# Kernel optimization log

Hardware: AMD Instinct MI355X
Metric: run time of the kernel (lower is better)

The kernel has to match this reference:

```python
import jax, jax.numpy as jnp
import numpy as np

N, K, D = 65536, 16, 64  # points, neighbors, d_out
EPS = 1e-5


def setup_inputs() -> dict:
    key = jax.random.key(0)
    ks = jax.random.split(key, 10)
    s = lambda fan: 1.0 / np.sqrt(fan)
    return {
        "p": jax.random.normal(ks[0], (N, K, 3), jnp.float32),
        "x": jax.random.normal(ks[1], (N, K, D), jnp.float32),
        # BiMLP: Conv1d(10, 2D, 1) -> BN -> ReLU -> Conv1d(2D, D, 1)
        "w1": jax.random.normal(ks[2], (10, 2 * D), jnp.float32) * s(10),
        "b1": jnp.zeros((2 * D,), jnp.float32),
        "g1": jnp.ones((2 * D,), jnp.float32),
        "be1": jnp.zeros((2 * D,), jnp.float32),
        "w2": jax.random.normal(ks[3], (2 * D, D), jnp.float32) * s(2 * D),
        "b2": jnp.zeros((D,), jnp.float32),
        # score_fn: Linear(2D, 2D, bias=False)
        "ws": jax.random.normal(ks[4], (2 * D, 2 * D), jnp.float32) * s(2 * D),
        # mlp_out: Linear(2D, D) -> BN -> ReLU
        "wo": jax.random.normal(ks[5], (2 * D, D), jnp.float32) * s(2 * D),
        "bo": jnp.zeros((D,), jnp.float32),
        "g2": jnp.ones((D,), jnp.float32),
        "be2": jnp.zeros((D,), jnp.float32),
    }


def reference(p, x, w1, b1, g1, be1, w2, b2, ws, wo, bo, g2, be2):
    # p: [N,K,3] neighbor coords (index 0 is the center), x: [N,K,D]
    center = p[:, :1, :]                                   # [N,1,3]
    diff = center - p                                      # [N,K,3]
    dist = jnp.sqrt(jnp.sum(diff * diff, axis=2, keepdims=True))  # [N,K,1]
    concat = jnp.concatenate(
        [jnp.broadcast_to(center, p.shape), p, diff, dist], axis=-1)  # [N,K,10]

    # 1x1 conv == per-point linear over channel dim
    h = jnp.einsum('nkc,cd->nkd', concat, w1) + b1          # [N,K,2D]
    # BatchNorm1d over (N,K) per channel (training-mode batch stats)
    mu = jnp.mean(h, axis=(0, 1))
    var = jnp.var(h, axis=(0, 1))
    h = (h - mu) * jax.lax.rsqrt(var + EPS) * g1 + be1
    h = jax.nn.relu(h)
    p_c = jnp.einsum('nkd,de->nke', h, w2) + b2             # [N,K,D]

    p_x = jnp.concatenate([p_c, x], axis=-1)                # [N,K,2D]
    # attention scores: linear (no bias) then softmax over neighbor dim (-2)
    scores = jax.nn.softmax(jnp.einsum('nkd,de->nke', p_x, ws), axis=-2)
    feat = jnp.sum(scores * p_x, axis=1)                    # [N,2D]

    out = feat @ wo + bo                                    # [N,D]
    mu2 = jnp.mean(out, axis=0)
    var2 = jnp.var(out, axis=0)
    out = (out - mu2) * jax.lax.rsqrt(var2 + EPS) * g2 + be2
    return jax.nn.relu(out)
```

## Files before the change

kernel.cpp:

```cpp
#include <hip/hip_runtime.h>
#include <math.h>

#define NPTS 65536
#define EPSV 1e-5f
#define B1G  256
#define B3G  512

#define OFF_P1  0
#define OFF_S1  (B1G*65)
#define OFF_P2  (OFF_S1+256)
#define OFF_S2  (OFF_P2+B3G*128)
#define OFF_PRE (OFF_S2+128)

typedef unsigned int u32;
typedef short v8s __attribute__((ext_vector_type(8)));
typedef float v4f __attribute__((ext_vector_type(4)));

union F8 { v8s v; u32 u[4]; unsigned short s[8]; };

__device__ __forceinline__ u32 f2bf(float f){
  u32 u = __float_as_uint(f);
  return (u + 0x7fffu + ((u>>16)&1u)) >> 16;
}
__device__ __forceinline__ float bf2f(unsigned short s){ return __uint_as_float(((u32)s)<<16); }
__device__ __forceinline__ u32 packbf(float a, float b){ return f2bf(a) | (f2bf(b)<<16); }

__global__ __launch_bounds__(256) void k1_stats(const float* __restrict__ p, float* __restrict__ part1){
  int tid = blockIdx.x*256 + threadIdx.x;
  float M[55]; float s[10];
  #pragma unroll
  for(int i=0;i<55;i++) M[i]=0.f;
  #pragma unroll
  for(int i=0;i<10;i++) s[i]=0.f;
  for(int it=0; it<16; ++it){
    int r = it*65536 + tid;
    int n = r >> 4;
    int kk = r & 15;
    const float* pn = p + (size_t)n*48;
    float cx=pn[0], cy=pn[1], cz=pn[2];
    float ax=pn[kk*3+0], ay=pn[kk*3+1], az=pn[kk*3+2];
    float dx=cx-ax, dy=cy-ay, dz=cz-az;
    float dd = sqrtf(dx*dx+dy*dy+dz*dz);
    float c[10]={cx,cy,cz,ax,ay,az,dx,dy,dz,dd};
    #pragma unroll
    for(int i=0;i<10;i++) s[i]+=c[i];
    int idx=0;
    #pragma unroll
    for(int i=0;i<10;i++){
      #pragma unroll
      for(int j=i;j<10;j++){
        M[idx] = fmaf(c[i],c[j],M[idx]);
        idx++;
      }
    }
  }
  #pragma unroll
  for(int i=0;i<10;i++){
    for(int off=32; off>0; off>>=1) s[i] += __shfl_down(s[i], off, 64);
  }
  #pragma unroll
  for(int i=0;i<55;i++){
    for(int off=32; off>0; off>>=1) M[i] += __shfl_down(M[i], off, 64);
  }
  __shared__ float sm[4][65];
  int lane = threadIdx.x & 63, w = threadIdx.x >> 6;
  if(lane==0){
    #pragma unroll
    for(int i=0;i<10;i++) sm[w][i]=s[i];
    #pragma unroll
    for(int i=0;i<55;i++) sm[w][10+i]=M[i];
  }
  __syncthreads();
  if(threadIdx.x<65){
    float v = sm[0][threadIdx.x]+sm[1][threadIdx.x]+sm[2][threadIdx.x]+sm[3][threadIdx.x];
    part1[blockIdx.x*65 + threadIdx.x] = v;
  }
}

__device__ __forceinline__ int tri_idx(int i,int j){
  int a = i<j? i : j;
  int b = i<j? j : i;
  return 10*a - (a*(a-1))/2 + (b-a);
}
__global__ void k2_fin(const float* __restrict__ part1, const float* __restrict__ w1,
                       const float* __restrict__ g1, const float* __restrict__ be1,
                       float* __restrict__ stats1){
  __shared__ float S[65];
  int t = threadIdx.x;
  if(t<65){
    float a=0.f;
    for(int b=0;b<B1G;b++) a += part1[b*65+t];
    S[t]=a;
  }
  __syncthreads();
  float wc[10];
  #pragma unroll
  for(int c=0;c<10;c++) wc[c]=w1[c*128+t];
  float md=0.f;
  #pragma unroll
  for(int c=0;c<10;c++) md += S[c]*wc[c];
  const float invR = 1.0f/(float)(NPTS*16);
  md *= invR;
  float q=0.f;
  #pragma unroll
  for(int i=0;i<10;i++){
    float ti=0.f;
    #pragma unroll
    for(int j=0;j<10;j++) ti += S[10+tri_idx(i,j)]*wc[j];
    q = fmaf(ti, wc[i], q);
  }
  q *= invR;
  float var = q - md*md;
  float sc = g1[t]*rsqrtf(var+EPSV);
  float sh = be1[t] - md*sc;
  stats1[t]=sc;
  stats1[128+t]=sh;
}

__global__ __launch_bounds__(256,2) void k3_main(
    const float* __restrict__ p, const float* __restrict__ x,
    const float* __restrict__ w2, const float* __restrict__ b2,
    const float* __restrict__ wsm, const float* __restrict__ wo,
    const float* __restrict__ w1, const float* __restrict__ stats1,
    float* __restrict__ pre, float* __restrict__ part2)
{
  __shared__ unsigned short s_h [4][16][136];
  __shared__ unsigned short s_px[4][16][136];
  __shared__ float          s_lg[4][16][132];
  __shared__ unsigned short s_ft[16][136];

  const int tid  = threadIdx.x;
  const int w    = tid>>6;
  const int lane = tid&63;
  const int q    = lane>>4;
  const int c    = lane&15;

  v8s Bw1[2], Bw2[4], Bws[2][4], Bwo[4];
  #pragma unroll
  for(int t=0;t<2;t++){
    F8 f;
    #pragma unroll
    for(int j=0;j<8;j++){
      int k = q*8+j;
      f.s[j] = (unsigned short)(k<10 ? f2bf(w1[k*128 + 32*w + 16*t + c]) : 0);
    }
    Bw1[t]=f.v;
  }
  #pragma unroll
  for(int kk=0;kk<4;kk++){
    F8 f;
    #pragma unroll
    for(int j=0;j<8;j++) f.s[j]=(unsigned short)f2bf(w2[(kk*32+q*8+j)*64 + 16*w + c]);
    Bw2[kk]=f.v;
  }
  #pragma unroll
  for(int t=0;t<2;t++){
    #pragma unroll
    for(int kk=0;kk<4;kk++){
      F8 f;
      #pragma unroll
      for(int j=0;j<8;j++) f.s[j]=(unsigned short)f2bf(wsm[(kk*32+q*8+j)*128 + 32*w + 16*t + c]);
      Bws[t][kk]=f.v;
    }
  }
  #pragma unroll
  for(int kk=0;kk<4;kk++){
    F8 f;
    #pragma unroll
    for(int j=0;j<8;j++) f.s[j]=(unsigned short)f2bf(wo[(kk*32+q*8+j)*64 + 16*w + c]);
    Bwo[kk]=f.v;
  }
  const float sc1a = stats1[32*w+c],    sh1a = stats1[128+32*w+c];
  const float sc1b = stats1[32*w+16+c], sh1b = stats1[128+32*w+16+c];
  const float b2v  = b2[16*w+c];

  float a_s=0.f, a_q=0.f;
  const int base0 = blockIdx.x*128;

  for(int r=0;r<32;++r){
    const int base = base0 + 4*r;

    const float4* xg = (const float4*)(x + (size_t)base*1024);
    #pragma unroll
    for(int rr=0;rr<4;rr++){
      int f = tid + 256*rr;
      float4 v = xg[f];
      int nl = f>>8, rem = f&255, pt = rem>>4, d4 = rem&15;
      *(uint2*)&s_px[nl][pt][64+4*d4] = make_uint2(packbf(v.x,v.y), packbf(v.z,v.w));
    }

    #pragma unroll
    for(int n0=0;n0<4;n0++){
      const float* pn = p + (size_t)(base+n0)*48;
      float cx=pn[0], cy=pn[1], cz=pn[2];
      float ax=pn[3*c], ay=pn[3*c+1], az=pn[3*c+2];
      float dx=cx-ax, dy=cy-ay, dz=cz-az;
      float dd=sqrtf(dx*dx+dy*dy+dz*dz);
      float cr[10]={cx,cy,cz,ax,ay,az,dx,dy,dz,dd};
      F8 fa;
      #pragma unroll
      for(int j=0;j<8;j++){ int k=q*8+j; fa.s[j]=(unsigned short)(k<10 ? f2bf(cr[k]) : 0); }
      v4f z={0.f,0.f,0.f,0.f};
      v4f d0 = __builtin_amdgcn_mfma_f32_16x16x32_bf16(fa.v, Bw1[0], z, 0,0,0);
      v4f d1 = __builtin_amdgcn_mfma_f32_16x16x32_bf16(fa.v, Bw1[1], z, 0,0,0);
      #pragma unroll
      for(int i=0;i<4;i++){
        float v0 = fmaxf(0.f, fmaf(d0[i], sc1a, sh1a));
        float v1 = fmaxf(0.f, fmaf(d1[i], sc1b, sh1b));
        s_h[n0][4*q+i][32*w+c]    = (unsigned short)f2bf(v0);
        s_h[n0][4*q+i][32*w+16+c] = (unsigned short)f2bf(v1);
      }
    }
    __syncthreads();

    #pragma unroll
    for(int n0=0;n0<4;n0++){
      const v8s* Ar = (const v8s*)&s_h[n0][c][0];
      v4f acc={0.f,0.f,0.f,0.f};
      #pragma unroll
      for(int kk=0;kk<4;kk++)
        acc = __builtin_amdgcn_mfma_f32_16x16x32_bf16(Ar[kk*4+q], Bw2[kk], acc, 0,0,0);
      #pragma unroll
      for(int i=0;i<4;i++) s_px[n0][4*q+i][16*w+c] = (unsigned short)f2bf(acc[i] + b2v);
    }
    __syncthreads();

    #pragma unroll
    for(int n0=0;n0<4;n0++){
      const v8s* Ar = (const v8s*)&s_px[n0][c][0];
      v4f l0={0.f,0.f,0.f,0.f}, l1={0.f,0.f,0.f,0.f};
      #pragma unroll
      for(int kk=0;kk<4;kk++){
        v8s a = Ar[kk*4+q];
        l0 = __builtin_amdgcn_mfma_f32_16x16x32_bf16(a, Bws[0][kk], l0, 0,0,0);
        l1 = __builtin_amdgcn_mfma_f32_16x16x32_bf16(a, Bws[1][kk], l1, 0,0,0);
      }
      #pragma unroll
      for(int i=0;i<4;i++){
        s_lg[n0][4*q+i][32*w+c]    = l0[i];
        s_lg[n0][4*q+i][32*w+16+c] = l1[i];
      }
    }
    __syncthreads();

    {
      const int slot = (r&3)*4 + w;
      #pragma unroll
      for(int hh=0;hh<2;hh++){
        const int ch = lane + 64*hh;
        float lv[16];
        #pragma unroll
        for(int pt=0;pt<16;pt++) lv[pt] = s_lg[w][pt][ch];
        float m = lv[0];
        #pragma unroll
        for(int pt=1;pt<16;pt++) m = fmaxf(m, lv[pt]);
        float se=0.f, fe=0.f;
        #pragma unroll
        for(int pt=0;pt<16;pt++){
          float e = __expf(lv[pt]-m);
          se += e;
          fe = fmaf(e, bf2f(s_px[w][pt][ch]), fe);
        }
        s_ft[slot][ch] = (unsigned short)f2bf(fe/se);
      }
    }
    __syncthreads();

    if((r&3)==3){
      const v8s* Ar = (const v8s*)&s_ft[c][0];
      v4f o={0.f,0.f,0.f,0.f};
      #pragma unroll
      for(int kk=0;kk<4;kk++)
        o = __builtin_amdgcn_mfma_f32_16x16x32_bf16(Ar[kk*4+q], Bwo[kk], o, 0,0,0);
      const int nb16 = base0 + (r>>2)*16;
      #pragma unroll
      for(int i=0;i<4;i++){
        float val = o[i];
        pre[(size_t)(nb16 + 4*q + i)*64 + 16*w + c] = val;
        a_s += val;
        a_q = fmaf(val,val,a_q);
      }
    }
  }

  a_s += __shfl_xor(a_s, 16, 64); a_s += __shfl_xor(a_s, 32, 64);
  a_q += __shfl_xor(a_q, 16, 64); a_q += __shfl_xor(a_q, 32, 64);
  if(q==0){
    part2[blockIdx.x*128 + 16*w + c]      = a_s;
    part2[blockIdx.x*128 + 64 + 16*w + c] = a_q;
  }
}

__global__ void k4_fin(const float* __restrict__ part2, const float* __restrict__ g2,
                       const float* __restrict__ be2, float* __restrict__ stats2){
  int t = threadIdx.x;
  float s=0.f, qq=0.f;
  for(int b=0;b<B3G;b++){ s += part2[b*128+t]; qq += part2[b*128+64+t]; }
  float mu  = s/(float)NPTS;
  float var = qq/(float)NPTS - mu*mu;
  float sc = g2[t]*rsqrtf(var+EPSV);
  float sh = be2[t] - mu*sc;
  stats2[t]=sc;
  stats2[64+t]=sh;
}

__global__ __launch_bounds__(256) void k5_apply(const float* __restrict__ pre,
                                                const float* __restrict__ stats2,
                                                float* __restrict__ out){
  int i = blockIdx.x*256 + threadIdx.x;
  float4 v = ((const float4*)pre)[i];
  int d4 = i & 15;
  float4 sc = ((const float4*)stats2)[d4];
  float4 sh = ((const float4*)(stats2+64))[d4];
  float4 o;
  o.x = fmaxf(0.f, fmaf(v.x,sc.x,sh.x));
  o.y = fmaxf(0.f, fmaf(v.y,sc.y,sh.y));
  o.z = fmaxf(0.f, fmaf(v.z,sc.z,sh.z));
  o.w = fmaxf(0.f, fmaf(v.w,sc.w,sh.w));
  ((float4*)out)[i] = o;
}

extern "C" void kernel_launch(void* const* d_in, const int* in_sizes, int n_in,
                              void* d_out, int out_size, void* d_ws, size_t ws_size,
                              hipStream_t stream){
  (void)in_sizes; (void)n_in; (void)out_size; (void)ws_size;
  const float* p   = (const float*)d_in[0];
  const float* x   = (const float*)d_in[1];
  const float* w1  = (const float*)d_in[2];
  const float* g1  = (const float*)d_in[4];
  const float* be1 = (const float*)d_in[5];
  const float* w2  = (const float*)d_in[6];
  const float* b2  = (const float*)d_in[7];
  const float* wsm = (const float*)d_in[8];
  const float* wo  = (const float*)d_in[9];
  const float* g2  = (const float*)d_in[11];
  const float* be2 = (const float*)d_in[12];

  float* wsf    = (float*)d_ws;
  float* part1  = wsf + OFF_P1;
  float* stats1 = wsf + OFF_S1;
  float* part2  = wsf + OFF_P2;
  float* stats2 = wsf + OFF_S2;
  float* pre    = wsf + OFF_PRE;
  float* out    = (float*)d_out;

  k1_stats<<<B1G,256,0,stream>>>(p, part1);
  k2_fin  <<<1,128,0,stream>>>(part1, w1, g1, be1, stats1);
  k3_main <<<B3G,256,0,stream>>>(p,x,w2,b2,wsm,wo,w1,stats1,pre,part2);
  k4_fin  <<<1,64,0,stream>>>(part2,g2,be2,stats2);
  k5_apply<<<4096,256,0,stream>>>(pre,stats2,out);
}
```

Measured before the change: 593.1 us.

## Fuse softmax into score MFMA epilogue, double k3 grid, parallelize finalize kernels

Softmax over neighbors is now computed directly from the MFMA score accumulators using cross-lane shuffles. This removes the float logit shared-memory buffer and one block barrier per iteration. The main kernel's grid doubles with half the points per block and a higher occupancy hint. Float-to-bf16 packing now uses the hardware v_cvt_pk_bf16_f32 instruction and division uses v_rcp_f32. Both reduction finalize kernels split their serial sums across more threads. Occupancy gains depend on register pressure fitting 4 blocks, and the fast reciprocal slightly changes rounding.

New measurement: 503.2 us. -15.1%, faster.

```diff
diff --git a/kernel.cpp b/kernel.cpp
--- a/kernel.cpp
+++ b/kernel.cpp
@@ -4,7 +4,7 @@
 #define NPTS 65536
 #define EPSV 1e-5f
 #define B1G  256
-#define B3G  512
+#define B3G  1024
 
 #define OFF_P1  0
 #define OFF_S1  (B1G*65)
@@ -23,7 +23,12 @@
   return (u + 0x7fffu + ((u>>16)&1u)) >> 16;
 }
 __device__ __forceinline__ float bf2f(unsigned short s){ return __uint_as_float(((u32)s)<<16); }
-__device__ __forceinline__ u32 packbf(float a, float b){ return f2bf(a) | (f2bf(b)<<16); }
+__device__ __forceinline__ u32 packbf(float a, float b){
+  u32 r; asm("v_cvt_pk_bf16_f32 %0, %1, %2" : "=v"(r) : "v"(a), "v"(b)); return r;
+}
+__device__ __forceinline__ float rcpf(float x){
+  float r; asm("v_rcp_f32 %0, %1" : "=v"(r) : "v"(x)); return r;
+}
 
 __global__ __launch_bounds__(256) void k1_stats(const float* __restrict__ p, float* __restrict__ part1){
   int tid = blockIdx.x*256 + threadIdx.x;
@@ -82,42 +87,48 @@
   int b = i<j? j : i;
   return 10*a - (a*(a-1))/2 + (b-a);
 }
-__global__ void k2_fin(const float* __restrict__ part1, const float* __restrict__ w1,
+__global__ __launch_bounds__(256) void k2_fin(const float* __restrict__ part1, const float* __restrict__ w1,
                        const float* __restrict__ g1, const float* __restrict__ be1,
                        float* __restrict__ stats1){
+  __shared__ float P[4][65];
   __shared__ float S[65];
   int t = threadIdx.x;
-  if(t<65){
+  for(int idx=t; idx<260; idx+=256){
+    int seg = idx/65, v = idx - seg*65;
     float a=0.f;
-    for(int b=0;b<B1G;b++) a += part1[b*65+t];
-    S[t]=a;
+    for(int b=seg; b<B1G; b+=4) a += part1[b*65+v];
+    P[seg][v]=a;
   }
   __syncthreads();
-  float wc[10];
-  #pragma unroll
-  for(int c=0;c<10;c++) wc[c]=w1[c*128+t];
-  float md=0.f;
-  #pragma unroll
-  for(int c=0;c<10;c++) md += S[c]*wc[c];
-  const float invR = 1.0f/(float)(NPTS*16);
-  md *= invR;
-  float q=0.f;
-  #pragma unroll
-  for(int i=0;i<10;i++){
-    float ti=0.f;
-    #pragma unroll
-    for(int j=0;j<10;j++) ti += S[10+tri_idx(i,j)]*wc[j];
-    q = fmaf(ti, wc[i], q);
-  }
-  q *= invR;
-  float var = q - md*md;
-  float sc = g1[t]*rsqrtf(var+EPSV);
-  float sh = be1[t] - md*sc;
-  stats1[t]=sc;
-  stats1[128+t]=sh;
-}
-
-__global__ __launch_bounds__(256,2) void k3_main(
+  if(t<65) S[t] = P[0][t]+P[1][t]+P[2][t]+P[3][t];
+  __syncthreads();
+  if(t<128){
+    float wc[10];
+    #pragma unroll
+    for(int c=0;c<10;c++) wc[c]=w1[c*128+t];
+    float md=0.f;
+    #pragma unroll
+    for(int c=0;c<10;c++) md += S[c]*wc[c];
+    const float invR = 1.0f/(float)(NPTS*16);
+    md *= invR;
+    float q=0.f;
+    #pragma unroll
+    for(int i=0;i<10;i++){
+      float ti=0.f;
+      #pragma unroll
+      for(int j=0;j<10;j++) ti += S[10+tri_idx(i,j)]*wc[j];
+      q = fmaf(ti, wc[i], q);
+    }
+    q *= invR;
+    float var = q - md*md;
+    float sc = g1[t]*rsqrtf(var+EPSV);
+    float sh = be1[t] - md*sc;
+    stats1[t]=sc;
+    stats1[128+t]=sh;
+  }
+}
+
+__global__ __launch_bounds__(256,4) void k3_main(
     const float* __restrict__ p, const float* __restrict__ x,
     const float* __restrict__ w2, const float* __restrict__ b2,
     const float* __restrict__ wsm, const float* __restrict__ wo,
@@ -126,7 +137,6 @@
 {
   __shared__ unsigned short s_h [4][16][136];
   __shared__ unsigned short s_px[4][16][136];
-  __shared__ float          s_lg[4][16][132];
   __shared__ unsigned short s_ft[16][136];
 
   const int tid  = threadIdx.x;
@@ -175,9 +185,9 @@
   const float b2v  = b2[16*w+c];
 
   float a_s=0.f, a_q=0.f;
-  const int base0 = blockIdx.x*128;
-
-  for(int r=0;r<32;++r){
+  const int base0 = blockIdx.x*64;
+
+  for(int r=0;r<16;++r){
     const int base = base0 + 4*r;
 
     const float4* xg = (const float4*)(x + (size_t)base*1024);
@@ -196,10 +206,13 @@
       float ax=pn[3*c], ay=pn[3*c+1], az=pn[3*c+2];
       float dx=cx-ax, dy=cy-ay, dz=cz-az;
       float dd=sqrtf(dx*dx+dy*dy+dz*dz);
-      float cr[10]={cx,cy,cz,ax,ay,az,dx,dy,dz,dd};
+      u32 pk01=packbf(cx,cy), pk23=packbf(cz,ax), pk45=packbf(ay,az),
+          pk67=packbf(dx,dy), pk89=packbf(dz,dd);
       F8 fa;
-      #pragma unroll
-      for(int j=0;j<8;j++){ int k=q*8+j; fa.s[j]=(unsigned short)(k<10 ? f2bf(cr[k]) : 0); }
+      fa.u[0] = q==0 ? pk01 : (q==1 ? pk89 : 0u);
+      fa.u[1] = q==0 ? pk23 : 0u;
+      fa.u[2] = q==0 ? pk45 : 0u;
+      fa.u[3] = q==0 ? pk67 : 0u;
       v4f z={0.f,0.f,0.f,0.f};
       v4f d0 = __builtin_amdgcn_mfma_f32_16x16x32_bf16(fa.v, Bw1[0], z, 0,0,0);
       v4f d1 = __builtin_amdgcn_mfma_f32_16x16x32_bf16(fa.v, Bw1[1], z, 0,0,0);
@@ -207,8 +220,9 @@
       for(int i=0;i<4;i++){
         float v0 = fmaxf(0.f, fmaf(d0[i], sc1a, sh1a));
         float v1 = fmaxf(0.f, fmaf(d1[i], sc1b, sh1b));
-        s_h[n0][4*q+i][32*w+c]    = (unsigned short)f2bf(v0);
-        s_h[n0][4*q+i][32*w+16+c] = (unsigned short)f2bf(v1);
+        u32 pk = packbf(v0, v1);
+        s_h[n0][4*q+i][32*w+c]    = (unsigned short)pk;
+        s_h[n0][4*q+i][32*w+16+c] = (unsigned short)(pk>>16);
       }
     }
     __syncthreads();
@@ -221,7 +235,11 @@
       for(int kk=0;kk<4;kk++)
         acc = __builtin_amdgcn_mfma_f32_16x16x32_bf16(Ar[kk*4+q], Bw2[kk], acc, 0,0,0);
       #pragma unroll
-      for(int i=0;i<4;i++) s_px[n0][4*q+i][16*w+c] = (unsigned short)f2bf(acc[i] + b2v);
+      for(int i=0;i<4;i+=2){
+        u32 pk = packbf(acc[i]+b2v, acc[i+1]+b2v);
+        s_px[n0][4*q+i][16*w+c]   = (unsigned short)pk;
+        s_px[n0][4*q+i+1][16*w+c] = (unsigned short)(pk>>16);
+      }
     }
     __syncthreads();
 
@@ -235,33 +253,31 @@
         l0 = __builtin_amdgcn_mfma_f32_16x16x32_bf16(a, Bws[0][kk], l0, 0,0,0);
         l1 = __builtin_amdgcn_mfma_f32_16x16x32_bf16(a, Bws[1][kk], l1, 0,0,0);
       }
+      float m0 = fmaxf(fmaxf(l0[0],l0[1]), fmaxf(l0[2],l0[3]));
+      float m1 = fmaxf(fmaxf(l1[0],l1[1]), fmaxf(l1[2],l1[3]));
+      m0 = fmaxf(m0, __shfl_xor(m0,16)); m0 = fmaxf(m0, __shfl_xor(m0,32));
+      m1 = fmaxf(m1, __shfl_xor(m1,16)); m1 = fmaxf(m1, __shfl_xor(m1,32));
+      float se0=0.f, se1=0.f, fe0=0.f, fe1=0.f;
       #pragma unroll
       for(int i=0;i<4;i++){
-        s_lg[n0][4*q+i][32*w+c]    = l0[i];
-        s_lg[n0][4*q+i][32*w+16+c] = l1[i];
-      }
-    }
-    __syncthreads();
-
-    {
-      const int slot = (r&3)*4 + w;
-      #pragma unroll
-      for(int hh=0;hh<2;hh++){
-        const int ch = lane + 64*hh;
-        float lv[16];
-        #pragma unroll
-        for(int pt=0;pt<16;pt++) lv[pt] = s_lg[w][pt][ch];
-        float m = lv[0];
-        #pragma unroll
-        for(int pt=1;pt<16;pt++) m = fmaxf(m, lv[pt]);
-        float se=0.f, fe=0.f;
-        #pragma unroll
-        for(int pt=0;pt<16;pt++){
-          float e = __expf(lv[pt]-m);
-          se += e;
-          fe = fmaf(e, bf2f(s_px[w][pt][ch]), fe);
-        }
-        s_ft[slot][ch] = (unsigned short)f2bf(fe/se);
+        int pt = 4*q+i;
+        float p0 = bf2f(s_px[n0][pt][32*w+c]);
+        float p1 = bf2f(s_px[n0][pt][32*w+16+c]);
+        float E0 = __expf(l0[i]-m0);
+        float E1 = __expf(l1[i]-m1);
+        se0 += E0; se1 += E1;
+        fe0 = fmaf(E0, p0, fe0);
+        fe1 = fmaf(E1, p1, fe1);
+      }
+      se0 += __shfl_xor(se0,16); se0 += __shfl_xor(se0,32);
+      se1 += __shfl_xor(se1,16); se1 += __shfl_xor(se1,32);
+      fe0 += __shfl_xor(fe0,16); fe0 += __shfl_xor(fe0,32);
+      fe1 += __shfl_xor(fe1,16); fe1 += __shfl_xor(fe1,32);
+      if(q==0){
+        u32 pk = packbf(fe0*rcpf(se0), fe1*rcpf(se1));
+        const int slot = (r&3)*4 + n0;
+        s_ft[slot][32*w+c]    = (unsigned short)pk;
+        s_ft[slot][32*w+16+c] = (unsigned short)(pk>>16);
       }
     }
     __syncthreads();
@@ -291,17 +307,31 @@
   }
 }
 
-__global__ void k4_fin(const float* __restrict__ part2, const float* __restrict__ g2,
+__global__ __launch_bounds__(512) void k4_fin(const float* __restrict__ part2, const float* __restrict__ g2,
                        const float* __restrict__ be2, float* __restrict__ stats2){
+  __shared__ float sm[8][128];
   int t = threadIdx.x;
+  int d = t & 63, seg = t >> 6;
   float s=0.f, qq=0.f;
-  for(int b=0;b<B3G;b++){ s += part2[b*128+t]; qq += part2[b*128+64+t]; }
-  float mu  = s/(float)NPTS;
-  float var = qq/(float)NPTS - mu*mu;
-  float sc = g2[t]*rsqrtf(var+EPSV);
-  float sh = be2[t] - mu*sc;
-  stats2[t]=sc;
-  stats2[64+t]=sh;
+  for(int i=0;i<B3G/8;i++){
+    int b = seg + 8*i;
+    s  += part2[b*128+d];
+    qq += part2[b*128+64+d];
+  }
+  sm[seg][d]    = s;
+  sm[seg][64+d] = qq;
+  __syncthreads();
+  if(t<64){
+    float S=0.f, Q=0.f;
+    #pragma unroll
+    for(int k=0;k<8;k++){ S += sm[k][t]; Q += sm[k][64+t]; }
+    float mu  = S/(float)NPTS;
+    float var = Q/(float)NPTS - mu*mu;
+    float sc = g2[t]*rsqrtf(var+EPSV);
+    float sh = be2[t] - mu*sc;
+    stats2[t]=sc;
+    stats2[64+t]=sh;
+  }
 }
 
 __global__ __launch_bounds__(256) void k5_apply(const float* __restrict__ pre,
@@ -345,8 +375,8 @@
   float* out    = (float*)d_out;
 
   k1_stats<<<B1G,256,0,stream>>>(p, part1);
-  k2_fin  <<<1,128,0,stream>>>(part1, w1, g1, be1, stats1);
+  k2_fin  <<<1,256,0,stream>>>(part1, w1, g1, be1, stats1);
   k3_main <<<B3G,256,0,stream>>>(p,x,w2,b2,wsm,wo,w1,stats1,pre,part2);
-  k4_fin  <<<1,64,0,stream>>>(part2,g2,be2,stats2);
+  k4_fin  <<<1,512,0,stream>>>(part2,g2,be2,stats2);
   k5_apply<<<4096,256,0,stream>>>(pre,stats2,out);
 }
```
